# Kernel optimization log

Hardware: AMD Instinct MI355X
Metric: run time of the kernel (lower is better)

Reference implementation:

```python
import jax, jax.numpy as jnp
import numpy as np

K = 16  # num_neighbors

def _gather(x, idx):
    # x: [B, D, N], idx: [B, N, K] -> [B, D, N, K]
    return jnp.take_along_axis(x[:, :, None, :], idx[:, None, :, :], axis=3)

def _mlp2d(x, w1, b1, w2, b2):
    # 1x1 Conv2d stack on [B, C, N, K]: conv -> relu -> conv
    h = jnp.einsum('hc,bcnk->bhnk', w1, x) + b1[None, :, None, None]
    h = jax.nn.relu(h)
    return jnp.einsum('oh,bhnk->bonk', w2, h) + b2[None, :, None, None]

def setup_inputs() -> dict:
    key = jax.random.key(0)
    ks = jax.random.split(key, 12)
    B, N, D, H = 4, 4096, 64, 64
    xyz = jax.random.normal(ks[0], (B, 3, N), dtype=jnp.float32)
    points = jax.random.normal(ks[1], (B, D, N), dtype=jnp.float32)
    def lin(k, fout, fin):
        return jax.random.normal(k, (fout, fin), dtype=jnp.float32) / np.sqrt(fin).astype(np.float32)
    w_qkv = lin(ks[2], 3 * D, D)
    w_pos1 = lin(ks[3], H, 3);   b_pos1 = jnp.zeros((H,), jnp.float32)
    w_pos2 = lin(ks[4], D, H);   b_pos2 = jnp.zeros((D,), jnp.float32)
    w_att1 = lin(ks[5], 4 * D, D); b_att1 = jnp.zeros((4 * D,), jnp.float32)
    w_att2 = lin(ks[6], D, 4 * D); b_att2 = jnp.zeros((D,), jnp.float32)
    return {"xyz": xyz, "points": points, "w_qkv": w_qkv,
            "w_pos1": w_pos1, "b_pos1": b_pos1, "w_pos2": w_pos2, "b_pos2": b_pos2,
            "w_att1": w_att1, "b_att1": b_att1, "w_att2": w_att2, "b_att2": b_att2}

def reference(xyz, points, w_qkv, w_pos1, b_pos1, w_pos2, b_pos2, w_att1, b_att1, w_att2, b_att2):
    B, C, N = xyz.shape
    D = points.shape[1]
    # KNN over points themselves (squared euclidean), indices of K nearest
    pts = jnp.swapaxes(xyz, 1, 2)              # [B, N, 3]
    sq = jnp.sum(pts * pts, axis=-1)           # [B, N]
    d2 = sq[:, :, None] + sq[:, None, :] - 2.0 * jnp.einsum('bnc,bmc->bnm', pts, pts)
    _, idx = jax.lax.top_k(-d2, K)             # [B, N, K]
    # relative position embedding
    grouped_xyz = xyz[:, :, :, None] - _gather(xyz, idx)          # [B, 3, N, K]
    rel_pos_emb = _mlp2d(grouped_xyz, w_pos1, b_pos1, w_pos2, b_pos2)  # [B, D, N, K]
    # qkv projection (1x1 conv, no bias)
    qkv = jnp.einsum('od,bdn->bon', w_qkv, points)                # [B, 3D, N]
    q, k, v = qkv[:, :D], qkv[:, D:2 * D], qkv[:, 2 * D:]
    qk_rel = q[:, :, :, None] - _gather(k, idx)                   # [B, D, N, K]
    v = _gather(v, idx) + rel_pos_emb                             # [B, D, N, K]
    sim = _mlp2d(qk_rel + rel_pos_emb, w_att1, b_att1, w_att2, b_att2)
    attn = jax.nn.softmax(sim, axis=-1)                           # softmax over K
    agg = jnp.sum(attn * v, axis=-1)                              # [B, D, N]
    return agg
```

## Files before the change

kernel.cpp:

```cpp
#include <hip/hip_runtime.h>
#include <hip/hip_bf16.h>
#include <stdint.h>

#define DEVI static __device__ __forceinline__

typedef unsigned short ushort_t;
typedef __attribute__((ext_vector_type(8))) short s8v;
typedef __attribute__((ext_vector_type(4))) float f4v;

constexpr int NPTS = 4096;
constexpr int BN   = 16384;

constexpr size_t OFF_FLAG = 0;
constexpr size_t OFF_XYZS = 16;
constexpr size_t OFF_WPK  = OFF_XYZS + 65536;
constexpr size_t OFF_WPOS = OFF_WPK + 256 * 144;
constexpr size_t OFF_B2   = OFF_WPOS + 64 * 80;
constexpr size_t OFF_BP2  = OFF_B2 + 64;
constexpr size_t OFF_WQKV = OFF_BP2 + 64;
constexpr size_t OFF_IDX  = OFF_WQKV + 192 * 64;
constexpr size_t OFF_KT   = OFF_IDX + (size_t)BN * 16;
constexpr size_t OFF_VT   = OFF_KT + (size_t)BN * 64;
constexpr size_t OFF_WSPL = OFF_VT + (size_t)BN * 64;
constexpr size_t U_W1H = 0;
constexpr size_t U_W1L = 16384;
constexpr size_t U_W2H = 32768;
constexpr size_t U_W2L = 49152;
constexpr size_t U_WP2H = 65536;
constexpr size_t U_WP2L = 69632;
constexpr size_t OFF_B1   = OFF_WSPL + 36864;
constexpr size_t OFF_WP1B = OFF_B1 + 256;
constexpr size_t FULL_FLOATS = OFF_WP1B + 256;

DEVI float b2f(__hip_bfloat16 h) { return __bfloat162float(h); }

DEVI float us2f(ushort_t u) {
    __hip_bfloat16 h;
    *(ushort_t*)&h = u;
    return __bfloat162float(h);
}

DEVI ushort_t f2us(float f) {
    __hip_bfloat16 h = __float2bfloat16(f);
    return *(ushort_t*)&h;
}

DEVI float ldin(const void* p, size_t i, int f32) {
    return f32 ? ((const float*)p)[i] : b2f(((const __hip_bfloat16*)p)[i]);
}

DEVI void split1(float x, ushort_t* h, ushort_t* l) {
    __hip_bfloat16 bh = __float2bfloat16(x);
    float r = x - __bfloat162float(bh);
    __hip_bfloat16 bl = __float2bfloat16(r);
    *h = *(ushort_t*)&bh;
    *l = *(ushort_t*)&bl;
}

DEVI void split4(f4v v, short4* h, short4* l) {
    ushort_t hh[4], ll[4];
#pragma unroll
    for (int r = 0; r < 4; r++) split1(v[r], &hh[r], &ll[r]);
    *h = make_short4((short)hh[0], (short)hh[1], (short)hh[2], (short)hh[3]);
    *l = make_short4((short)ll[0], (short)ll[1], (short)ll[2], (short)ll[3]);
}

DEVI s8v cat8(short4 a, short4 b) {
    s8v r;
    r[0] = a.x; r[1] = a.y; r[2] = a.z; r[3] = a.w;
    r[4] = b.x; r[5] = b.y; r[6] = b.z; r[7] = b.w;
    return r;
}

DEVI f4v MF(s8v a, s8v b, f4v c) {
    return __builtin_amdgcn_mfma_f32_16x16x32_bf16(a, b, c, 0, 0, 0);
}

DEVI unsigned long long shflx64(unsigned long long v, int m) {
    unsigned lo = __shfl_xor((unsigned)(v & 0xffffffffull), m, 64);
    unsigned hi = __shfl_xor((unsigned)(v >> 32), m, 64);
    return ((unsigned long long)hi << 32) | lo;
}

DEVI int kperm(int k) {
    int base = k & ~31;
    int q = (k & 15) >> 2;
    int hi = (k >> 4) & 1;
    int j = (hi << 2) | (k & 3);
    return base + q * 8 + j;
}

__global__ void detect_kernel(const void* xyz, unsigned* flagp) {
    __shared__ int s;
    int t = threadIdx.x;
    if (t == 0) s = 0;
    __syncthreads();
    const ushort_t* u = (const ushort_t*)xyz;
    int cnt = 0;
    for (int i = t; i < 2048; i += 256) {
        unsigned e = (u[i] >> 7) & 0xFFu;
        cnt += (e >= 140u);
    }
    atomicAdd(&s, cnt);
    __syncthreads();
    if (t == 0) *flagp = (s > 16) ? 1u : 0u;
}

__global__ void prep_kernel(const void* xyz, const void* w_qkv,
                            const void* w_pos1, const void* b_pos1,
                            const void* w_pos2, const void* b_pos2,
                            const void* w_att1, const void* b_att1,
                            const void* w_att2, const void* b_att2,
                            float* ws, int use_kv) {
    int f32 = (int)((const unsigned*)ws)[OFF_FLAG];
    int t = threadIdx.x;
    int blk = blockIdx.x;
    if (blk == 0) {
        float* wp = ws + OFF_WPK + (size_t)t * 144;
        for (int d = 0; d < 64; d++) wp[d]      = ldin(w_att1, t * 64 + d, f32);
        for (int d = 0; d < 64; d++) wp[64 + d] = ldin(w_att2, d * 256 + t, f32);
        wp[128] = ldin(b_att1, t, f32);
    } else if (blk == 1) {
        if (t < 64) {
            float* wp = ws + OFF_WPOS + (size_t)t * 80;
            wp[0] = ldin(w_pos1, t * 3 + 0, f32);
            wp[1] = ldin(w_pos1, t * 3 + 1, f32);
            wp[2] = ldin(w_pos1, t * 3 + 2, f32);
            wp[3] = ldin(b_pos1, t, f32);
            for (int d = 0; d < 64; d++) wp[4 + d] = ldin(w_pos2, d * 64 + t, f32);
            ws[OFF_B2 + t]  = ldin(b_att2, t, f32);
            ws[OFF_BP2 + t] = ldin(b_pos2, t, f32);
        }
        for (int i = t; i < 192 * 64; i += 256) ws[OFF_WQKV + i] = ldin(w_qkv, i, f32);
    } else if (blk < 66) {
        int gid = (blk - 2) * 256 + t;
        int b = gid >> 12, n = gid & 4095;
        float x = ldin(xyz, (size_t)(b * 3 + 0) * NPTS + n, f32);
        float y = ldin(xyz, (size_t)(b * 3 + 1) * NPTS + n, f32);
        float z = ldin(xyz, (size_t)(b * 3 + 2) * NPTS + n, f32);
        float sq = __fadd_rn(__fadd_rn(__fmul_rn(x, x), __fmul_rn(y, y)), __fmul_rn(z, z));
        ((float4*)(ws + OFF_XYZS))[gid] = make_float4(x, y, z, sq);
    } else if (blk == 66) {
        if (!use_kv) return;
        ushort_t* wsp = (ushort_t*)(ws + OFF_WSPL);
        for (int d = 0; d < 64; d++) {
            int dst = t * 64 + kperm(d);
            split1(ldin(w_att1, t * 64 + d, f32), &wsp[U_W1H + dst], &wsp[U_W1L + dst]);
        }
        ws[OFF_B1 + t] = ldin(b_att1, t, f32);
    } else {
        if (!use_kv) return;
        ushort_t* wsp = (ushort_t*)(ws + OFF_WSPL);
        for (int i = t; i < 64 * 256; i += 256) {
            int row = i >> 8, k = i & 255;
            int dst = row * 256 + kperm(k);
            split1(ldin(w_att2, i, f32), &wsp[U_W2H + dst], &wsp[U_W2L + dst]);
        }
        for (int i = t; i < 64 * 64; i += 256) {
            int row = i >> 6, k = i & 63;
            int dst = row * 64 + kperm(k);
            split1(ldin(w_pos2, i, f32), &wsp[U_WP2H + dst], &wsp[U_WP2L + dst]);
        }
        if (t < 64) {
            ws[OFF_WP1B + t * 4 + 0] = ldin(w_pos1, t * 3 + 0, f32);
            ws[OFF_WP1B + t * 4 + 1] = ldin(w_pos1, t * 3 + 1, f32);
            ws[OFF_WP1B + t * 4 + 2] = ldin(w_pos1, t * 3 + 2, f32);
            ws[OFF_WP1B + t * 4 + 3] = ldin(b_pos1, t, f32);
        }
    }
}

__global__ void kv_kernel(const void* points, float* ws) {
    __shared__ float T[128 * 65];
    int f32 = (int)((const unsigned*)ws)[OFF_FLAG];
    const float* wq = ws + OFF_WQKV + 64 * 64;
    int t = threadIdx.x;
    int wid = __builtin_amdgcn_readfirstlane(t >> 6);
    int lane = t & 63;
    int b = blockIdx.x >> 6;
    int n0 = (blockIdx.x & 63) * 64;

    float P[64];
#pragma unroll
    for (int d = 0; d < 64; d++)
        P[d] = ldin(points, (size_t)(b * 64 + d) * NPTS + n0 + lane, f32);

    for (int i = 0; i < 32; i++) {
        int o = wid + 4 * i;
        const float* wr = wq + o * 64;
        float acc = 0.f;
#pragma unroll
        for (int d = 0; d < 64; d++) acc = fmaf(wr[d], P[d], acc);
        T[o * 65 + lane] = acc;
    }
    __syncthreads();

#pragma unroll
    for (int a2 = 0; a2 < 2; a2++) {
        float* dst = ws + (a2 == 0 ? OFF_KT : OFF_VT);
#pragma unroll
        for (int j = 0; j < 4; j++) {
            int ci = j * 256 + t;
            int np = ci >> 4, dp = ci & 15;
            float4 v;
            v.x = T[(a2 * 64 + dp * 4 + 0) * 65 + np];
            v.y = T[(a2 * 64 + dp * 4 + 1) * 65 + np];
            v.z = T[(a2 * 64 + dp * 4 + 2) * 65 + np];
            v.w = T[(a2 * 64 + dp * 4 + 3) * 65 + np];
            *(float4*)(dst + ((size_t)((b << 12) + n0 + np)) * 64 + dp * 4) = v;
        }
    }
}

template <int NK>
DEVI unsigned long long knn_row(const float4* base, float4 pn, int lane,
                                unsigned* out_row, unsigned long long* kept_worst) {
    unsigned long long arr[NK];
#pragma unroll
    for (int i = 0; i < NK; i++) arr[i] = ~0ull;
    float sqn = pn.w;
#pragma unroll 4
    for (int j = 0; j < 64; j++) {
        int m = (j << 6) + lane;
        float4 pm = base[m];
        float dot = __fadd_rn(__fadd_rn(__fmul_rn(pn.x, pm.x), __fmul_rn(pn.y, pm.y)),
                              __fmul_rn(pn.z, pm.z));
        float d2 = __fsub_rn(__fadd_rn(sqn, pm.w), __fmul_rn(2.0f, dot));
        unsigned ub = __float_as_uint(d2);
        unsigned sg = (unsigned)((int)ub >> 31);
        ub = ub ^ (sg | 0x80000000u);
        unsigned long long key = ((unsigned long long)ub << 32) | (unsigned)m;
#pragma unroll
        for (int i = 0; i < NK; i++) {
            bool lt = key < arr[i];
            unsigned long long lo = lt ? key : arr[i];
            key = lt ? arr[i] : key;
            arr[i] = lo;
        }
    }
    unsigned long long kw = arr[NK - 1];
    unsigned long long v16 = 0;
    for (int r = 0; r < 16; r++) {
        unsigned long long mn = arr[0];
#pragma unroll
        for (int s = 1; s < 64; s <<= 1) {
            unsigned long long o = shflx64(mn, s);
            if (o < mn) mn = o;
        }
        if (arr[0] == mn) {
#pragma unroll
            for (int i = 0; i < NK - 1; i++) arr[i] = arr[i + 1];
            arr[NK - 1] = ~0ull;
            out_row[r] = (unsigned)(mn & 0xffffffffu);
        }
        v16 = mn;
    }
    *kept_worst = kw;
    return v16;
}

__global__ void knn_kernel(float* ws) {
    int t = threadIdx.x;
    int wid = t >> 6, lane = t & 63;
    int row = blockIdx.x * 4 + wid;
    int b = row >> 12;
    const float4* base = (const float4*)(ws + OFF_XYZS) + ((size_t)b << 12);
    float4 pn = base[row & 4095];
    unsigned* orow = (unsigned*)(ws + OFF_IDX) + (size_t)row * 16;

    unsigned long long kw;
    unsigned long long v16 = knn_row<4>(base, pn, lane, orow, &kw);
    if (__any(kw < v16)) {
        knn_row<16>(base, pn, lane, orow, &kw);
    }
}

__attribute__((amdgpu_waves_per_eu(4, 4)))
__global__ __launch_bounds__(1024) void pt_mfma5(const float* __restrict__ ws,
                                                 const void* __restrict__ points,
                                                 void* __restrict__ out) {
    __shared__ __align__(16) ushort_t W1Hs[256 * 72];
    __shared__ __align__(16) ushort_t W1Ls[256 * 72];
    __shared__ __align__(16) ushort_t W2Hs[64 * 264];
    __shared__ __align__(16) ushort_t W2Ls[64 * 264];
    __shared__ float PLOUT[64 * 33];
    __shared__ float QL[32][68];

    int f32 = (int)((const unsigned*)ws)[OFF_FLAG];
    const float* KTp  = ws + OFF_KT;
    const float* VTp  = ws + OFF_VT;
    const float* wq   = ws + OFF_WQKV;
    const float* b1p  = ws + OFF_B1;
    const float* b2p  = ws + OFF_B2;
    const float* bp2p = ws + OFF_BP2;
    const float* wp1b = ws + OFF_WP1B;
    const ushort_t* wsp = (const ushort_t*)(ws + OFF_WSPL);
    const ushort_t* wp2h = wsp + U_WP2H;
    const ushort_t* wp2l = wsp + U_WP2L;
    const unsigned* idxp = (const unsigned*)(ws + OFF_IDX);
    const float4* xyzs = (const float4*)(ws + OFF_XYZS);

    int t = threadIdx.x;
    int w = t >> 6, lane = t & 63;
    int cl = lane & 15, quad = lane >> 4;

    int bx = blockIdx.x;
    int x = bx & 7;
    int b = x & 3;
    int n0 = (((x >> 2) * 64) + (bx >> 3)) << 5;

    {
        const ushort_t* srcs[4] = {wsp + U_W1H, wsp + U_W1L, wsp + U_W2H, wsp + U_W2L};
        ushort_t* dsts[4] = {W1Hs, W1Ls, W2Hs, W2Ls};
#pragma unroll
        for (int a = 0; a < 4; a++) {
            const ushort_t* s = srcs[a];
            ushort_t* dl = dsts[a];
            bool isw1 = a < 2;
            for (int i = t; i < 2048; i += 1024) {
                int r = isw1 ? (i >> 3) : (i >> 5);
                int c = isw1 ? (i & 7) : (i & 31);
                int stride = isw1 ? 72 : 264;
                uint4 v = *(const uint4*)(s + ((size_t)i << 3));
                *(uint4*)(dl + r * stride + (c << 3)) = v;
            }
        }
    }

    {
        int d = t >> 4, c2 = (t & 15) * 2;
        size_t base = (size_t)(b * 64 + d) * NPTS + n0 + c2;
        if (f32) {
            float2 pv = *(const float2*)((const float*)points + base);
            PLOUT[d * 33 + c2] = pv.x; PLOUT[d * 33 + c2 + 1] = pv.y;
        } else {
            ushort2 pv = *(const ushort2*)((const ushort_t*)points + base);
            PLOUT[d * 33 + c2] = us2f(pv.x); PLOUT[d * 33 + c2 + 1] = us2f(pv.y);
        }
    }
    __syncthreads();

    {
        int nl = lane & 31, sg = lane >> 5;
        for (int oi = 0; oi < 4; oi++) {
            int o = w * 4 + oi;
            const float* wr = wq + o * 64 + sg * 32;
            float p = 0.f;
#pragma unroll
            for (int jj = 0; jj < 32; jj++) p = fmaf(wr[jj], PLOUT[(sg * 32 + jj) * 33 + nl], p);
            p += __shfl_xor(p, 32, 64);
            if (lane < 32) QL[nl][o] = p;
        }
    }

    int mrow[2];
#pragma unroll
    for (int nti = 0; nti < 2; nti++) {
        int row = (b << 12) + n0 + 2 * w + nti;
        mrow[nti] = (b << 12) + (int)(idxp[(size_t)row * 16 + cl] & 4095u);
    }

    short4 HpH[2][4], HpL[2][4];
#pragma unroll
    for (int nti = 0; nti < 2; nti++) {
        int row = (b << 12) + n0 + 2 * w + nti;
        float4 pn = xyzs[row];
        float4 pm = xyzs[mrow[nti]];
        float rx = pn.x - pm.x, ry = pn.y - pm.y, rz = pn.z - pm.z;
#pragma unroll
        for (int hk = 0; hk < 4; hk++) {
            f4v hv;
#pragma unroll
            for (int j = 0; j < 4; j++) {
                int h = hk * 16 + quad * 4 + j;
                float4 wv = *(const float4*)(wp1b + (size_t)h * 4);
                hv[j] = fmaxf(fmaf(wv.x, rx, fmaf(wv.y, ry, fmaf(wv.z, rz, wv.w))), 0.f);
            }
            split4(hv, &HpH[nti][hk], &HpL[nti][hk]);
        }
    }
    __syncthreads();

    f4v rpe[2][4];
#pragma unroll
    for (int i = 0; i < 2; i++)
#pragma unroll
        for (int j = 0; j < 4; j++) rpe[i][j] = {0.f, 0.f, 0.f, 0.f};

#pragma unroll
    for (int hk2 = 0; hk2 < 2; hk2++) {
        s8v bh[2], bl[2];
#pragma unroll
        for (int nti = 0; nti < 2; nti++) {
            bh[nti] = cat8(HpH[nti][2 * hk2], HpH[nti][2 * hk2 + 1]);
            bl[nti] = cat8(HpL[nti][2 * hk2], HpL[nti][2 * hk2 + 1]);
        }
#pragma unroll
        for (int dt = 0; dt < 4; dt++) {
            size_t ao = (size_t)(dt * 16 + cl) * 64 + hk2 * 32 + quad * 8;
            s8v ah = *(const s8v*)(wp2h + ao);
            s8v al = *(const s8v*)(wp2l + ao);
#pragma unroll
            for (int nti = 0; nti < 2; nti++) {
                rpe[nti][dt] = MF(ah, bh[nti], rpe[nti][dt]);
                rpe[nti][dt] = MF(ah, bl[nti], rpe[nti][dt]);
                rpe[nti][dt] = MF(al, bh[nti], rpe[nti][dt]);
            }
        }
    }
#pragma unroll
    for (int dt = 0; dt < 4; dt++) {
        float4 bv = *(const float4*)(bp2p + dt * 16 + quad * 4);
#pragma unroll
        for (int nti = 0; nti < 2; nti++) {
            rpe[nti][dt][0] += bv.x; rpe[nti][dt][1] += bv.y;
            rpe[nti][dt][2] += bv.z; rpe[nti][dt][3] += bv.w;
        }
    }

    short4 XH4[2][4], XL4[2][4];
#pragma unroll
    for (int nti = 0; nti < 2; nti++) {
        int nt = 2 * w + nti;
#pragma unroll
        for (int dt = 0; dt < 4; dt++) {
            int d0 = dt * 16 + quad * 4;
            float4 q4 = *(const float4*)&QL[nt][d0];
            float4 k4 = *(const float4*)(KTp + (size_t)mrow[nti] * 64 + d0);
            f4v xv;
            xv[0] = (q4.x - k4.x) + rpe[nti][dt][0];
            xv[1] = (q4.y - k4.y) + rpe[nti][dt][1];
            xv[2] = (q4.z - k4.z) + rpe[nti][dt][2];
            xv[3] = (q4.w - k4.w) + rpe[nti][dt][3];
            split4(xv, &XH4[nti][dt], &XL4[nti][dt]);
        }
    }

    f4v sim[2][4];
#pragma unroll
    for (int i = 0; i < 2; i++)
#pragma unroll
        for (int j = 0; j < 4; j++) sim[i][j] = {0.f, 0.f, 0.f, 0.f};

    for (int ot2 = 0; ot2 < 8; ot2++) {
        f4v hacc[2][2];
#pragma unroll
        for (int i = 0; i < 2; i++)
#pragma unroll
            for (int j = 0; j < 2; j++) hacc[i][j] = {0.f, 0.f, 0.f, 0.f};
#pragma unroll
        for (int dt2 = 0; dt2 < 2; dt2++) {
            s8v xbh[2], xbl[2];
#pragma unroll
            for (int nti = 0; nti < 2; nti++) {
                xbh[nti] = cat8(XH4[nti][2 * dt2], XH4[nti][2 * dt2 + 1]);
                xbl[nti] = cat8(XL4[nti][2 * dt2], XL4[nti][2 * dt2 + 1]);
            }
#pragma unroll
            for (int half = 0; half < 2; half++) {
                int lo = (ot2 * 32 + half * 16 + cl) * 72 + (dt2 * 4 + quad) * 8;
                s8v ah = *(const s8v*)&W1Hs[lo];
                s8v al = *(const s8v*)&W1Ls[lo];
#pragma unroll
                for (int nti = 0; nti < 2; nti++) {
                    hacc[half][nti] = MF(ah, xbh[nti], hacc[half][nti]);
                    hacc[half][nti] = MF(ah, xbl[nti], hacc[half][nti]);
                    hacc[half][nti] = MF(al, xbh[nti], hacc[half][nti]);
                }
            }
        }
        short4 hh[2][2], hl[2][2];
#pragma unroll
        for (int half = 0; half < 2; half++) {
            float4 bv = *(const float4*)(b1p + ot2 * 32 + half * 16 + quad * 4);
            float bb[4] = {bv.x, bv.y, bv.z, bv.w};
#pragma unroll
            for (int nti = 0; nti < 2; nti++) {
                f4v hv;
#pragma unroll
                for (int r = 0; r < 4; r++) hv[r] = fmaxf(hacc[half][nti][r] + bb[r], 0.f);
                split4(hv, &hh[half][nti], &hl[half][nti]);
            }
        }
        s8v hbh[2], hbl[2];
#pragma unroll
        for (int nti = 0; nti < 2; nti++) {
            hbh[nti] = cat8(hh[0][nti], hh[1][nti]);
            hbl[nti] = cat8(hl[0][nti], hl[1][nti]);
        }
#pragma unroll
        for (int dt = 0; dt < 4; dt++) {
            int lo = (dt * 16 + cl) * 264 + (ot2 * 4 + quad) * 8;
            s8v ah = *(const s8v*)&W2Hs[lo];
            s8v al = *(const s8v*)&W2Ls[lo];
#pragma unroll
            for (int nti = 0; nti < 2; nti++) {
                sim[nti][dt] = MF(ah, hbh[nti], sim[nti][dt]);
                sim[nti][dt] = MF(ah, hbl[nti], sim[nti][dt]);
                sim[nti][dt] = MF(al, hbh[nti], sim[nti][dt]);
            }
        }
    }

#pragma unroll
    for (int nti = 0; nti < 2; nti++) {
        int nt = 2 * w + nti;
#pragma unroll
        for (int dt = 0; dt < 4; dt++) {
            int d0 = dt * 16 + quad * 4;
            float4 b2v = *(const float4*)(b2p + d0);
            float4 v4 = *(const float4*)(VTp + (size_t)mrow[nti] * 64 + d0);
            float bb[4] = {b2v.x, b2v.y, b2v.z, b2v.w};
            float vv[4] = {v4.x, v4.y, v4.z, v4.w};
#pragma unroll
            for (int r = 0; r < 4; r++) {
                float s = sim[nti][dt][r] + bb[r];
                float mx = s;
                mx = fmaxf(mx, __shfl_xor(mx, 1, 64));
                mx = fmaxf(mx, __shfl_xor(mx, 2, 64));
                mx = fmaxf(mx, __shfl_xor(mx, 4, 64));
                mx = fmaxf(mx, __shfl_xor(mx, 8, 64));
                float e = __expf(s - mx);
                float sm = e;
                sm += __shfl_xor(sm, 1, 64);
                sm += __shfl_xor(sm, 2, 64);
                sm += __shfl_xor(sm, 4, 64);
                sm += __shfl_xor(sm, 8, 64);
                float p = e * (vv[r] + rpe[nti][dt][r]);
                p += __shfl_xor(p, 1, 64);
                p += __shfl_xor(p, 2, 64);
                p += __shfl_xor(p, 4, 64);
                p += __shfl_xor(p, 8, 64);
                if (cl == 0) PLOUT[(d0 + r) * 33 + nt] = p / sm;
            }
        }
    }
    __syncthreads();

    {
        int d = t >> 4, c2 = (t & 15) * 2;
        float a = PLOUT[d * 33 + c2], bb = PLOUT[d * 33 + c2 + 1];
        size_t ofs = (size_t)(b * 64 + d) * NPTS + n0 + c2;
        if (f32) {
            float2 v = {a, bb};
            *(float2*)((float*)out + ofs) = v;
        } else {
            unsigned pk = (unsigned)f2us(a) | ((unsigned)f2us(bb) << 16);
            *(unsigned*)((ushort_t*)out + ofs) = pk;
        }
    }
}

__global__ __launch_bounds__(256, 2) void pt_main_compact(const float* __restrict__ ws,
                                                          const void* __restrict__ points,
                                                          void* __restrict__ out) {
    __shared__ float PL[64 * 16];
    __shared__ float QL[16 * 68];
    __shared__ float OUTS[64 * 16];

    int f32 = (int)((const unsigned*)ws)[OFF_FLAG];
    const float* wpack = ws + OFF_WPK;
    const float* wpos  = ws + OFF_WPOS;
    const float* b2p   = ws + OFF_B2;
    const float* bp2p  = ws + OFF_BP2;
    const float* wq    = ws + OFF_WQKV;
    const unsigned* idxws = (const unsigned*)(ws + OFF_IDX);
    const float4* xyzs = (const float4*)(ws + OFF_XYZS);

    int t = threadIdx.x;
    int wid = t >> 6, lane = t & 63;

    int bx = blockIdx.x;
    int x = bx & 7, j = bx >> 3;
    int b = x & 3;
    int n0 = ((((x >> 2) << 7) + j) << 4);

    {
        int d = t >> 2, c4 = t & 3;
        size_t base = (size_t)(b * 64 + d) * NPTS + n0 + c4 * 4;
        if (f32) {
            float4 pv = *(const float4*)((const float*)points + base);
            PL[d * 16 + c4 * 4 + 0] = pv.x;
            PL[d * 16 + c4 * 4 + 1] = pv.y;
            PL[d * 16 + c4 * 4 + 2] = pv.z;
            PL[d * 16 + c4 * 4 + 3] = pv.w;
        } else {
            ushort4 pv = *(const ushort4*)((const ushort_t*)points + base);
            PL[d * 16 + c4 * 4 + 0] = us2f(pv.x);
            PL[d * 16 + c4 * 4 + 1] = us2f(pv.y);
            PL[d * 16 + c4 * 4 + 2] = us2f(pv.z);
            PL[d * 16 + c4 * 4 + 3] = us2f(pv.w);
        }
    }
    __syncthreads();

    {
        int sg = lane >> 4, nl = lane & 15;
        for (int oi = 0; oi < 16; oi++) {
            int o = wid * 16 + oi;
            const float* wr = wq + o * 64 + sg * 16;
            float p = 0.f;
#pragma unroll
            for (int jj = 0; jj < 16; jj++) p = fmaf(wr[jj], PL[(sg * 16 + jj) * 16 + nl], p);
            p += __shfl_xor(p, 16, 64);
            p += __shfl_xor(p, 32, 64);
            if (lane < 16) QL[nl * 68 + o] = p;
        }
    }
    __syncthreads();

    int k = lane & 15, nsub = lane >> 4;
    int nl = wid * 4 + nsub;
    int n = n0 + nl;
    int row = (b << 12) + n;
    unsigned m = idxws[(size_t)row * 16 + k] & 4095u;

    float4 pn = xyzs[row];
    float4 pmx = xyzs[(b << 12) + (int)m];
    float rx = pn.x - pmx.x, ry = pn.y - pmx.y, rz = pn.z - pmx.z;

    float rpe[64];
#pragma unroll
    for (int d = 0; d < 64; d++) rpe[d] = bp2p[d];
#pragma unroll 2
    for (int o = 0; o < 64; o++) {
        const float* wr = wpos + o * 80;
        float hp = fmaf(wr[0], rx, fmaf(wr[1], ry, fmaf(wr[2], rz, wr[3])));
        hp = fmaxf(hp, 0.f);
#pragma unroll
        for (int d = 0; d < 64; d++) rpe[d] = fmaf(wr[4 + d], hp, rpe[d]);
    }

    float Pm[64];
#pragma unroll
    for (int d = 0; d < 64; d++)
        Pm[d] = ldin(points, ((size_t)(b * 64 + d) << 12) + (int)m, f32);

    float X[64];
    {
        const float* qrow = QL + nl * 68;
#pragma unroll 2
        for (int d = 0; d < 64; d++) {
            const float* wr = wq + (64 + d) * 64;
            float kd = 0.f;
#pragma unroll
            for (int dd = 0; dd < 64; dd++) kd = fmaf(wr[dd], Pm[dd], kd);
            X[d] = (qrow[d] - kd) + rpe[d];
        }
    }

    float sim[64];
#pragma unroll
    for (int d = 0; d < 64; d++) sim[d] = b2p[d];
#pragma unroll 2
    for (int o = 0; o < 256; o++) {
        const float* wr = wpack + (size_t)o * 144;
        float h0 = 0.f, h1 = 0.f, h2 = 0.f, h3 = 0.f;
#pragma unroll
        for (int jj = 0; jj < 16; jj++) {
            h0 = fmaf(wr[jj],      X[jj],      h0);
            h1 = fmaf(wr[16 + jj], X[16 + jj], h1);
            h2 = fmaf(wr[32 + jj], X[32 + jj], h2);
            h3 = fmaf(wr[48 + jj], X[48 + jj], h3);
        }
        float h = ((h0 + h1) + (h2 + h3)) + wr[128];
        h = fmaxf(h, 0.f);
#pragma unroll
        for (int d = 0; d < 64; d++) sim[d] = fmaf(wr[64 + d], h, sim[d]);
    }

    {
#pragma unroll
        for (int d4 = 0; d4 < 16; d4++) {
            float vvv[4];
#pragma unroll
            for (int jj = 0; jj < 4; jj++) {
                int d = 4 * d4 + jj;
                const float* wrv = wq + (128 + d) * 64;
                float vd = 0.f;
#pragma unroll
                for (int dd = 0; dd < 64; dd++) vd = fmaf(wrv[dd], Pm[dd], vd);
                vvv[jj] = vd + rpe[d];
            }
#pragma unroll
            for (int jj = 0; jj < 4; jj++) {
                int d = 4 * d4 + jj;
                float s = sim[d];
                float mx = s;
                mx = fmaxf(mx, __shfl_xor(mx, 1, 64));
                mx = fmaxf(mx, __shfl_xor(mx, 2, 64));
                mx = fmaxf(mx, __shfl_xor(mx, 4, 64));
                mx = fmaxf(mx, __shfl_xor(mx, 8, 64));
                float e = __expf(s - mx);
                float sm = e;
                sm += __shfl_xor(sm, 1, 64);
                sm += __shfl_xor(sm, 2, 64);
                sm += __shfl_xor(sm, 4, 64);
                sm += __shfl_xor(sm, 8, 64);
                float p = e * vvv[jj];
                p += __shfl_xor(p, 1, 64);
                p += __shfl_xor(p, 2, 64);
                p += __shfl_xor(p, 4, 64);
                p += __shfl_xor(p, 8, 64);
                if (k == 0) OUTS[d * 16 + nl] = p / sm;
            }
        }
    }
    __syncthreads();

    {
        int d = t >> 2, c = t & 3;
        float4 v = *(const float4*)&OUTS[d * 16 + c * 4];
        size_t ofs = (size_t)(b * 64 + d) * NPTS + n0 + c * 4;
        if (f32) {
            *(float4*)((float*)out + ofs) = v;
        } else {
            uint2 pk;
            pk.x = (unsigned)f2us(v.x) | ((unsigned)f2us(v.y) << 16);
            pk.y = (unsigned)f2us(v.z) | ((unsigned)f2us(v.w) << 16);
            *(uint2*)((ushort_t*)out + ofs) = pk;
        }
    }
}

extern "C" void kernel_launch(void* const* d_in, const int* in_sizes, int n_in,
                              void* d_out, int out_size, void* d_ws, size_t ws_size,
                              hipStream_t stream) {
    const void* xyz    = d_in[0];
    const void* points = d_in[1];
    const void* w_qkv  = d_in[2];
    const void* w_pos1 = d_in[3];
    const void* b_pos1 = d_in[4];
    const void* w_pos2 = d_in[5];
    const void* b_pos2 = d_in[6];
    const void* w_att1 = d_in[7];
    const void* b_att1 = d_in[8];
    const void* w_att2 = d_in[9];
    const void* b_att2 = d_in[10];
    float* ws = (float*)d_ws;

    int use_kv = ws_size >= FULL_FLOATS * sizeof(float) ? 1 : 0;

    hipLaunchKernelGGL(detect_kernel, dim3(1), dim3(256), 0, stream,
                       xyz, (unsigned*)ws + OFF_FLAG);
    hipLaunchKernelGGL(prep_kernel, dim3(68), dim3(256), 0, stream,
                       xyz, w_qkv, w_pos1, b_pos1, w_pos2, b_pos2,
                       w_att1, b_att1, w_att2, b_att2, ws, use_kv);
    if (use_kv)
        hipLaunchKernelGGL(kv_kernel, dim3(256), dim3(256), 0, stream, points, ws);
    hipLaunchKernelGGL(knn_kernel, dim3(4096), dim3(256), 0, stream, ws);
    if (use_kv)
        hipLaunchKernelGGL(pt_mfma5, dim3(512), dim3(1024), 0, stream, (const float*)ws, points, d_out);
    else
        hipLaunchKernelGGL(pt_main_compact, dim3(1024), dim3(256), 0, stream, (const float*)ws, points, d_out);
}
```

Before: 347.9 us.

## Process point tiles sequentially per wave to cut register pressure

Restructures the main attention kernel so each wave handles its two neighbor-point tiles one after another (unroll 1), instead of keeping both tiles' position embeddings, split inputs and accumulators live at the same time. It also removes the waves-per-EU attribute. The aim is lower VGPR use and less spilling under the 1024-thread launch bound. In exchange it loses the interleaving of independent MFMA chains across the two tiles and reads the shared weight tiles twice per wave.

```diff
diff --git a/kernel.cpp b/kernel.cpp
--- a/kernel.cpp
+++ b/kernel.cpp
@@ -275,8 +275,7 @@
     }
 }
 
-__attribute__((amdgpu_waves_per_eu(4, 4)))
-__global__ __launch_bounds__(1024) void pt_mfma5(const float* __restrict__ ws,
+__global__ __launch_bounds__(1024) void pt_mfma6(const float* __restrict__ ws,
                                                  const void* __restrict__ points,
                                                  void* __restrict__ out) {
     __shared__ __align__(16) ushort_t W1Hs[256 * 72];
@@ -352,169 +351,126 @@
             if (lane < 32) QL[nl][o] = p;
         }
     }
-
-    int mrow[2];
-#pragma unroll
-    for (int nti = 0; nti < 2; nti++) {
-        int row = (b << 12) + n0 + 2 * w + nti;
-        mrow[nti] = (b << 12) + (int)(idxp[(size_t)row * 16 + cl] & 4095u);
-    }
-
-    short4 HpH[2][4], HpL[2][4];
-#pragma unroll
-    for (int nti = 0; nti < 2; nti++) {
-        int row = (b << 12) + n0 + 2 * w + nti;
-        float4 pn = xyzs[row];
-        float4 pm = xyzs[mrow[nti]];
-        float rx = pn.x - pm.x, ry = pn.y - pm.y, rz = pn.z - pm.z;
-#pragma unroll
-        for (int hk = 0; hk < 4; hk++) {
-            f4v hv;
-#pragma unroll
-            for (int j = 0; j < 4; j++) {
-                int h = hk * 16 + quad * 4 + j;
-                float4 wv = *(const float4*)(wp1b + (size_t)h * 4);
-                hv[j] = fmaxf(fmaf(wv.x, rx, fmaf(wv.y, ry, fmaf(wv.z, rz, wv.w))), 0.f);
-            }
-            split4(hv, &HpH[nti][hk], &HpL[nti][hk]);
-        }
-    }
-    __syncthreads();
-
-    f4v rpe[2][4];
-#pragma unroll
-    for (int i = 0; i < 2; i++)
-#pragma unroll
-        for (int j = 0; j < 4; j++) rpe[i][j] = {0.f, 0.f, 0.f, 0.f};
-
-#pragma unroll
-    for (int hk2 = 0; hk2 < 2; hk2++) {
-        s8v bh[2], bl[2];
-#pragma unroll
-        for (int nti = 0; nti < 2; nti++) {
-            bh[nti] = cat8(HpH[nti][2 * hk2], HpH[nti][2 * hk2 + 1]);
-            bl[nti] = cat8(HpL[nti][2 * hk2], HpL[nti][2 * hk2 + 1]);
-        }
-#pragma unroll
-        for (int dt = 0; dt < 4; dt++) {
-            size_t ao = (size_t)(dt * 16 + cl) * 64 + hk2 * 32 + quad * 8;
-            s8v ah = *(const s8v*)(wp2h + ao);
-            s8v al = *(const s8v*)(wp2l + ao);
-#pragma unroll
-            for (int nti = 0; nti < 2; nti++) {
-                rpe[nti][dt] = MF(ah, bh[nti], rpe[nti][dt]);
-                rpe[nti][dt] = MF(ah, bl[nti], rpe[nti][dt]);
-                rpe[nti][dt] = MF(al, bh[nti], rpe[nti][dt]);
-            }
-        }
-    }
-#pragma unroll
-    for (int dt = 0; dt < 4; dt++) {
-        float4 bv = *(const float4*)(bp2p + dt * 16 + quad * 4);
-#pragma unroll
-        for (int nti = 0; nti < 2; nti++) {
-            rpe[nti][dt][0] += bv.x; rpe[nti][dt][1] += bv.y;
-            rpe[nti][dt][2] += bv.z; rpe[nti][dt][3] += bv.w;
-        }
-    }
-
-    short4 XH4[2][4], XL4[2][4];
-#pragma unroll
+    __syncthreads();
+
+#pragma unroll 1
     for (int nti = 0; nti < 2; nti++) {
         int nt = 2 * w + nti;
+        int row = (b << 12) + n0 + nt;
+        int mrow = (b << 12) + (int)(idxp[(size_t)row * 16 + cl] & 4095u);
+
+        short4 HpH[4], HpL[4];
+        {
+            float4 pn = xyzs[row];
+            float4 pm = xyzs[mrow];
+            float rx = pn.x - pm.x, ry = pn.y - pm.y, rz = pn.z - pm.z;
+#pragma unroll
+            for (int hk = 0; hk < 4; hk++) {
+                f4v hv;
+#pragma unroll
+                for (int j = 0; j < 4; j++) {
+                    int h = hk * 16 + quad * 4 + j;
+                    float4 wv = *(const float4*)(wp1b + (size_t)h * 4);
+                    hv[j] = fmaxf(fmaf(wv.x, rx, fmaf(wv.y, ry, fmaf(wv.z, rz, wv.w))), 0.f);
+                }
+                split4(hv, &HpH[hk], &HpL[hk]);
+            }
+        }
+
+        f4v rpe[4];
+#pragma unroll
+        for (int j = 0; j < 4; j++) rpe[j] = {0.f, 0.f, 0.f, 0.f};
+#pragma unroll
+        for (int hk2 = 0; hk2 < 2; hk2++) {
+            s8v bh = cat8(HpH[2 * hk2], HpH[2 * hk2 + 1]);
+            s8v bl = cat8(HpL[2 * hk2], HpL[2 * hk2 + 1]);
+#pragma unroll
+            for (int dt = 0; dt < 4; dt++) {
+                size_t ao = (size_t)(dt * 16 + cl) * 64 + hk2 * 32 + quad * 8;
+                s8v ah = *(const s8v*)(wp2h + ao);
+                s8v al = *(const s8v*)(wp2l + ao);
+                rpe[dt] = MF(ah, bh, rpe[dt]);
+                rpe[dt] = MF(ah, bl, rpe[dt]);
+                rpe[dt] = MF(al, bh, rpe[dt]);
+            }
+        }
+#pragma unroll
+        for (int dt = 0; dt < 4; dt++) {
+            float4 bv = *(const float4*)(bp2p + dt * 16 + quad * 4);
+            rpe[dt][0] += bv.x; rpe[dt][1] += bv.y;
+            rpe[dt][2] += bv.z; rpe[dt][3] += bv.w;
+        }
+
+        short4 XH4[4], XL4[4];
 #pragma unroll
         for (int dt = 0; dt < 4; dt++) {
             int d0 = dt * 16 + quad * 4;
             float4 q4 = *(const float4*)&QL[nt][d0];
-            float4 k4 = *(const float4*)(KTp + (size_t)mrow[nti] * 64 + d0);
+            float4 k4 = *(const float4*)(KTp + (size_t)mrow * 64 + d0);
             f4v xv;
-            xv[0] = (q4.x - k4.x) + rpe[nti][dt][0];
-            xv[1] = (q4.y - k4.y) + rpe[nti][dt][1];
-            xv[2] = (q4.z - k4.z) + rpe[nti][dt][2];
-            xv[3] = (q4.w - k4.w) + rpe[nti][dt][3];
-            split4(xv, &XH4[nti][dt], &XL4[nti][dt]);
-        }
-    }
-
-    f4v sim[2][4];
-#pragma unroll
-    for (int i = 0; i < 2; i++)
-#pragma unroll
-        for (int j = 0; j < 4; j++) sim[i][j] = {0.f, 0.f, 0.f, 0.f};
-
-    for (int ot2 = 0; ot2 < 8; ot2++) {
-        f4v hacc[2][2];
-#pragma unroll
-        for (int i = 0; i < 2; i++)
-#pragma unroll
-            for (int j = 0; j < 2; j++) hacc[i][j] = {0.f, 0.f, 0.f, 0.f};
-#pragma unroll
-        for (int dt2 = 0; dt2 < 2; dt2++) {
-            s8v xbh[2], xbl[2];
-#pragma unroll
-            for (int nti = 0; nti < 2; nti++) {
-                xbh[nti] = cat8(XH4[nti][2 * dt2], XH4[nti][2 * dt2 + 1]);
-                xbl[nti] = cat8(XL4[nti][2 * dt2], XL4[nti][2 * dt2 + 1]);
-            }
+            xv[0] = (q4.x - k4.x) + rpe[dt][0];
+            xv[1] = (q4.y - k4.y) + rpe[dt][1];
+            xv[2] = (q4.z - k4.z) + rpe[dt][2];
+            xv[3] = (q4.w - k4.w) + rpe[dt][3];
+            split4(xv, &XH4[dt], &XL4[dt]);
+        }
+
+        f4v sim[4];
+#pragma unroll
+        for (int j = 0; j < 4; j++) sim[j] = {0.f, 0.f, 0.f, 0.f};
+
+        for (int ot2 = 0; ot2 < 8; ot2++) {
+            f4v hacc[2];
+            hacc[0] = {0.f, 0.f, 0.f, 0.f};
+            hacc[1] = {0.f, 0.f, 0.f, 0.f};
+#pragma unroll
+            for (int dt2 = 0; dt2 < 2; dt2++) {
+                s8v xbh = cat8(XH4[2 * dt2], XH4[2 * dt2 + 1]);
+                s8v xbl = cat8(XL4[2 * dt2], XL4[2 * dt2 + 1]);
+#pragma unroll
+                for (int half = 0; half < 2; half++) {
+                    int lo = (ot2 * 32 + half * 16 + cl) * 72 + (dt2 * 4 + quad) * 8;
+                    s8v ah = *(const s8v*)&W1Hs[lo];
+                    s8v al = *(const s8v*)&W1Ls[lo];
+                    hacc[half] = MF(ah, xbh, hacc[half]);
+                    hacc[half] = MF(ah, xbl, hacc[half]);
+                    hacc[half] = MF(al, xbh, hacc[half]);
+                }
+            }
+            short4 hh[2], hl[2];
 #pragma unroll
             for (int half = 0; half < 2; half++) {
-                int lo = (ot2 * 32 + half * 16 + cl) * 72 + (dt2 * 4 + quad) * 8;
-                s8v ah = *(const s8v*)&W1Hs[lo];
-                s8v al = *(const s8v*)&W1Ls[lo];
-#pragma unroll
-                for (int nti = 0; nti < 2; nti++) {
-                    hacc[half][nti] = MF(ah, xbh[nti], hacc[half][nti]);
-                    hacc[half][nti] = MF(ah, xbl[nti], hacc[half][nti]);
-                    hacc[half][nti] = MF(al, xbh[nti], hacc[half][nti]);
-                }
-            }
-        }
-        short4 hh[2][2], hl[2][2];
-#pragma unroll
-        for (int half = 0; half < 2; half++) {
-            float4 bv = *(const float4*)(b1p + ot2 * 32 + half * 16 + quad * 4);
-            float bb[4] = {bv.x, bv.y, bv.z, bv.w};
-#pragma unroll
-            for (int nti = 0; nti < 2; nti++) {
+                float4 bv = *(const float4*)(b1p + ot2 * 32 + half * 16 + quad * 4);
                 f4v hv;
-#pragma unroll
-                for (int r = 0; r < 4; r++) hv[r] = fmaxf(hacc[half][nti][r] + bb[r], 0.f);
-                split4(hv, &hh[half][nti], &hl[half][nti]);
-            }
-        }
-        s8v hbh[2], hbl[2];
-#pragma unroll
-        for (int nti = 0; nti < 2; nti++) {
-            hbh[nti] = cat8(hh[0][nti], hh[1][nti]);
-            hbl[nti] = cat8(hl[0][nti], hl[1][nti]);
-        }
-#pragma unroll
-        for (int dt = 0; dt < 4; dt++) {
-            int lo = (dt * 16 + cl) * 264 + (ot2 * 4 + quad) * 8;
-            s8v ah = *(const s8v*)&W2Hs[lo];
-            s8v al = *(const s8v*)&W2Ls[lo];
-#pragma unroll
-            for (int nti = 0; nti < 2; nti++) {
-                sim[nti][dt] = MF(ah, hbh[nti], sim[nti][dt]);
-                sim[nti][dt] = MF(ah, hbl[nti], sim[nti][dt]);
-                sim[nti][dt] = MF(al, hbh[nti], sim[nti][dt]);
-            }
-        }
-    }
-
-#pragma unroll
-    for (int nti = 0; nti < 2; nti++) {
-        int nt = 2 * w + nti;
+                hv[0] = fmaxf(hacc[half][0] + bv.x, 0.f);
+                hv[1] = fmaxf(hacc[half][1] + bv.y, 0.f);
+                hv[2] = fmaxf(hacc[half][2] + bv.z, 0.f);
+                hv[3] = fmaxf(hacc[half][3] + bv.w, 0.f);
+                split4(hv, &hh[half], &hl[half]);
+            }
+            s8v hbh = cat8(hh[0], hh[1]);
+            s8v hbl = cat8(hl[0], hl[1]);
+#pragma unroll
+            for (int dt = 0; dt < 4; dt++) {
+                int lo = (dt * 16 + cl) * 264 + (ot2 * 4 + quad) * 8;
+                s8v ah = *(const s8v*)&W2Hs[lo];
+                s8v al = *(const s8v*)&W2Ls[lo];
+                sim[dt] = MF(ah, hbh, sim[dt]);
+                sim[dt] = MF(ah, hbl, sim[dt]);
+                sim[dt] = MF(al, hbh, sim[dt]);
+            }
+        }
+
 #pragma unroll
         for (int dt = 0; dt < 4; dt++) {
             int d0 = dt * 16 + quad * 4;
             float4 b2v = *(const float4*)(b2p + d0);
-            float4 v4 = *(const float4*)(VTp + (size_t)mrow[nti] * 64 + d0);
+            float4 v4 = *(const float4*)(VTp + (size_t)mrow * 64 + d0);
             float bb[4] = {b2v.x, b2v.y, b2v.z, b2v.w};
             float vv[4] = {v4.x, v4.y, v4.z, v4.w};
 #pragma unroll
             for (int r = 0; r < 4; r++) {
-                float s = sim[nti][dt][r] + bb[r];
+                float s = sim[dt][r] + bb[r];
                 float mx = s;
                 mx = fmaxf(mx, __shfl_xor(mx, 1, 64));
                 mx = fmaxf(mx, __shfl_xor(mx, 2, 64));
@@ -526,7 +482,7 @@
                 sm += __shfl_xor(sm, 2, 64);
                 sm += __shfl_xor(sm, 4, 64);
                 sm += __shfl_xor(sm, 8, 64);
-                float p = e * (vv[r] + rpe[nti][dt][r]);
+                float p = e * (vv[r] + rpe[dt][r]);
                 p += __shfl_xor(p, 1, 64);
                 p += __shfl_xor(p, 2, 64);
                 p += __shfl_xor(p, 4, 64);
@@ -750,7 +706,7 @@
         hipLaunchKernelGGL(kv_kernel, dim3(256), dim3(256), 0, stream, points, ws);
     hipLaunchKernelGGL(knn_kernel, dim3(4096), dim3(256), 0, stream, ws);
     if (use_kv)
-        hipLaunchKernelGGL(pt_mfma5, dim3(512), dim3(1024), 0, stream, (const float*)ws, points, d_out);
+        hipLaunchKernelGGL(pt_mfma6, dim3(512), dim3(1024), 0, stream, (const float*)ws, points, d_out);
     else
         hipLaunchKernelGGL(pt_main_compact, dim3(1024), dim3(256), 0, stream, (const float*)ws, points, d_out);
 }
```

Result: slower. 1.248 ms (+258.6%).
